# Performance work log

Hardware: AMD Instinct MI355X
Metric: run time of the kernel (lower is better)

Reference implementation:

```python
import jax, jax.numpy as jnp
import numpy as np

N, E, F_IN, C, H = 50000, 800000, 256, 128, 2
NEG_SLOPE = 0.2


def setup_inputs() -> dict:
    key = jax.random.key(0)
    ks = jax.random.split(key, 8)
    x = jax.random.normal(ks[0], (N, F_IN), dtype=jnp.float32)
    edge_index = jax.random.randint(ks[1], (2, E), 0, N, dtype=jnp.int64)
    # GATConv params (PyG: lin weight [H*C, F_IN], att_src/att_dst [H, C], bias [H*C])
    s_lin = 1.0 / np.sqrt(F_IN)
    W = jax.random.uniform(ks[2], (H * C, F_IN), minval=-s_lin, maxval=s_lin, dtype=jnp.float32)
    att_src = jax.random.normal(ks[3], (H, C), dtype=jnp.float32) * 0.1
    att_dst = jax.random.normal(ks[4], (H, C), dtype=jnp.float32) * 0.1
    bias = jnp.zeros((H * C,), dtype=jnp.float32)
    # trailing nn.Linear(H*C, C)
    s_l = 1.0 / np.sqrt(H * C)
    lin_w = jax.random.uniform(ks[5], (C, H * C), minval=-s_l, maxval=s_l, dtype=jnp.float32)
    lin_b = jax.random.uniform(ks[6], (C,), minval=-s_l, maxval=s_l, dtype=jnp.float32)
    return {"x": x, "edge_index": edge_index, "W": W, "att_src": att_src,
            "att_dst": att_dst, "bias": bias, "lin_w": lin_w, "lin_b": lin_b}


def _gat_forward(x, edge_index, W, att_src, att_dst, bias, lin_w, lin_b):
    # add self-loops (PyG default add_self_loops=True)
    loop = jnp.arange(N, dtype=edge_index.dtype)
    src = jnp.concatenate([edge_index[0], loop])  # [E+N]
    dst = jnp.concatenate([edge_index[1], loop])  # [E+N]

    h = (x @ W.T).reshape(N, H, C)                # [N, H, C]
    a_src = jnp.einsum('nhc,hc->nh', h, att_src)  # [N, H]
    a_dst = jnp.einsum('nhc,hc->nh', h, att_dst)  # [N, H]

    e = a_src[src] + a_dst[dst]                   # [E+N, H]
    e = jnp.where(e > 0, e, NEG_SLOPE * e)        # LeakyReLU(0.2)

    # softmax over edges grouped by destination node
    m = jax.ops.segment_max(e, dst, num_segments=N)          # [N, H]
    m = jnp.where(jnp.isfinite(m), m, 0.0)
    ex = jnp.exp(e - jax.lax.stop_gradient(m)[dst])
    denom = jax.ops.segment_sum(ex, dst, num_segments=N)     # [N, H]
    alpha = ex / jnp.maximum(denom[dst], 1e-16)               # [E+N, H]

    msg = h[src] * alpha[:, :, None]                          # [E+N, H, C]
    out = jax.ops.segment_sum(msg, dst, num_segments=N)       # [N, H, C]
    out = out.reshape(N, H * C) + bias

    out = jax.nn.elu(out)
    return out @ lin_w.T + lin_b                               # [N, C]


def reference(x, edge_index, W, att_src, att_dst, bias, lin_w, lin_b):
    return _gat_forward(x, edge_index, W, att_src, att_dst, bias, lin_w, lin_b)
```

## Files before the change

### kernel.cpp

```cpp
#include <hip/hip_runtime.h>
#include <hip/hip_fp16.h>
#include <math.h>

#define NN 50000
#define EE 800000
#define ET (EE + NN)
#define FIN 256
#define CCOUT 128
#define HH 2
#define HC 256
#define NEG 0.2f

#define NB_EDGE ((ET + 255) / 256)
#define NB_SCAN ((NN + 255) / 256)
#define NB_XPREP (NN / 4)

#define PREP_W_BLOCKS 64
#define PREP_LW_BLOCKS 32
#define PREP_GRID (3 + PREP_W_BLOCKS + PREP_LW_BLOCKS)

typedef __attribute__((ext_vector_type(8))) short short8;
typedef __attribute__((ext_vector_type(4))) float floatx4;

__device__ __forceinline__ unsigned short f2bf(float f)
{
    union { float f; unsigned int u; } x; x.f = f;
    unsigned int r = x.u + 0x7fffu + ((x.u >> 16) & 1u);
    return (unsigned short)(r >> 16);
}
__device__ __forceinline__ float bf2f(unsigned short u)
{
    union { unsigned int u; float f; } x; x.u = ((unsigned int)u) << 16;
    return x.f;
}
__device__ __forceinline__ float h2f_bits(unsigned short u)
{
    __half h = *(const __half*)&u;
    return __half2float(h);
}

__device__ __forceinline__ int load_idx(const int* ei32, int is64, int pos)
{
    return is64 ? ei32[2 * pos] : ei32[pos];
}

__global__ __launch_bounds__(256) void prep_kernel(const float* __restrict__ W,
                                                   const float* __restrict__ att_s,
                                                   const float* __restrict__ att_d,
                                                   const float* __restrict__ lin_w,
                                                   const int* __restrict__ ei32,
                                                   float* __restrict__ was,
                                                   float* __restrict__ wad,
                                                   unsigned short* __restrict__ Wb,
                                                   unsigned short* __restrict__ linwb,
                                                   int* __restrict__ flag)
{
    int b = blockIdx.x, t = threadIdx.x;
    if (b == 0) {
        if (t < 64) {
            int v = ei32[2 * t + 1];
            unsigned long long m = __ballot(v != 0);
            if (t == 0) *flag = (m == 0ull) ? 1 : 0;
        }
    } else if (b <= 2) {
        int hd = b - 1;
        float as = 0.f, ad = 0.f;
        for (int c = 0; c < CCOUT; c++) {
            float wv = W[(size_t)(hd * CCOUT + c) * FIN + t];
            as += att_s[hd * CCOUT + c] * wv;
            ad += att_d[hd * CCOUT + c] * wv;
        }
        was[hd * FIN + t] = as;
        wad[hd * FIN + t] = ad;
    } else if (b < 3 + PREP_W_BLOCKS) {
        int i = (b - 3) * 256 + t;
        float4 v = *(const float4*)(W + (size_t)i * 4);
        ushort4 o;
        o.x = f2bf(v.x); o.y = f2bf(v.y); o.z = f2bf(v.z); o.w = f2bf(v.w);
        *(ushort4*)(Wb + (size_t)i * 4) = o;
    } else {
        int i = (b - 3 - PREP_W_BLOCKS) * 256 + t;
        float4 v = *(const float4*)(lin_w + (size_t)i * 4);
        ushort4 o;
        o.x = f2bf(v.x); o.y = f2bf(v.y); o.z = f2bf(v.z); o.w = f2bf(v.w);
        *(ushort4*)(linwb + (size_t)i * 4) = o;
    }
}

__global__ __launch_bounds__(256) void xprep_count_kernel(const float* __restrict__ x,
                                                          const float* __restrict__ was,
                                                          const float* __restrict__ wad,
                                                          unsigned short* __restrict__ xb,
                                                          float* __restrict__ a_s,
                                                          float* __restrict__ a_d,
                                                          const int* __restrict__ ei32,
                                                          const int* __restrict__ flag,
                                                          int* __restrict__ deg,
                                                          int* __restrict__ eord)
{
    int b = blockIdx.x, t = threadIdx.x;
    if (b < NB_XPREP) {
        int w = t >> 6, l = t & 63;
        int n = b * 4 + w;
        float4 xv = *(const float4*)(x + (size_t)n * FIN + l * 4);
        ushort4 xs;
        xs.x = f2bf(xv.x); xs.y = f2bf(xv.y); xs.z = f2bf(xv.z); xs.w = f2bf(xv.w);
        *(ushort4*)(xb + (size_t)n * FIN + l * 4) = xs;

        float4 s0 = *(const float4*)(was + l * 4);
        float4 s1 = *(const float4*)(was + FIN + l * 4);
        float4 d0 = *(const float4*)(wad + l * 4);
        float4 d1 = *(const float4*)(wad + FIN + l * 4);
        float vs0 = xv.x * s0.x + xv.y * s0.y + xv.z * s0.z + xv.w * s0.w;
        float vs1 = xv.x * s1.x + xv.y * s1.y + xv.z * s1.z + xv.w * s1.w;
        float vd0 = xv.x * d0.x + xv.y * d0.y + xv.z * d0.z + xv.w * d0.w;
        float vd1 = xv.x * d1.x + xv.y * d1.y + xv.z * d1.z + xv.w * d1.w;
#pragma unroll
        for (int off = 32; off > 0; off >>= 1) {
            vs0 += __shfl_down(vs0, off);
            vs1 += __shfl_down(vs1, off);
            vd0 += __shfl_down(vd0, off);
            vd1 += __shfl_down(vd1, off);
        }
        if (l == 0) {
            a_s[n * 2 + 0] = vs0; a_s[n * 2 + 1] = vs1;
            a_d[n * 2 + 0] = vd0; a_d[n * 2 + 1] = vd1;
        }
    } else {
        int e = (b - NB_XPREP) * 256 + t;
        if (e < ET) {
            int is64 = *flag;
            int d = (e < EE) ? load_idx(ei32, is64, EE + e) : (e - EE);
            eord[e] = atomicAdd(&deg[d], 1);
        }
    }
}

template <bool ADD_BIAS, bool OUT_BF16>
__global__ __launch_bounds__(256) void gemm_mfma(const unsigned short* __restrict__ A,
                                                 const unsigned short* __restrict__ B,
                                                 const float* __restrict__ bias,
                                                 void* __restrict__ Cout,
                                                 int M, int N, int K)
{
    const int LDT = 40;
    __shared__ unsigned short As[128 * LDT];
    __shared__ unsigned short Bs[128 * LDT];

    int tid = threadIdx.x;
    int wave = tid >> 6, lane = tid & 63;
    int wr = wave >> 1, wc = wave & 1;
    int quad = lane >> 4, l16 = lane & 15;
    int bm0 = blockIdx.x * 128;
    int bn0 = blockIdx.y * 128;

    floatx4 acc[4][4] = {};

    for (int kk = 0; kk < K; kk += 32) {
#pragma unroll
        for (int p = 0; p < 2; p++) {
            int idx = p * 256 + tid;
            int row = idx >> 2, seg = idx & 3;
            int grow = bm0 + row; if (grow >= M) grow = M - 1;
            uint4 va = *(const uint4*)(A + (size_t)grow * K + kk + seg * 8);
            *(uint4*)(&As[row * LDT + seg * 8]) = va;
            uint4 vb = *(const uint4*)(B + (size_t)(bn0 + row) * K + kk + seg * 8);
            *(uint4*)(&Bs[row * LDT + seg * 8]) = vb;
        }
        __syncthreads();

        short8 af[4], bfr[4];
#pragma unroll
        for (int mi = 0; mi < 4; mi++)
            af[mi] = *(const short8*)(&As[(wr * 64 + mi * 16 + l16) * LDT + quad * 8]);
#pragma unroll
        for (int ni = 0; ni < 4; ni++)
            bfr[ni] = *(const short8*)(&Bs[(wc * 64 + ni * 16 + l16) * LDT + quad * 8]);
#pragma unroll
        for (int mi = 0; mi < 4; mi++)
#pragma unroll
            for (int ni = 0; ni < 4; ni++)
                acc[mi][ni] = __builtin_amdgcn_mfma_f32_16x16x32_bf16(af[mi], bfr[ni], acc[mi][ni], 0, 0, 0);
        __syncthreads();
    }

#pragma unroll
    for (int mi = 0; mi < 4; mi++) {
#pragma unroll
        for (int ni = 0; ni < 4; ni++) {
            int col = bn0 + wc * 64 + ni * 16 + l16;
#pragma unroll
            for (int r = 0; r < 4; r++) {
                int row = bm0 + wr * 64 + mi * 16 + quad * 4 + r;
                if (row < M) {
                    float v = acc[mi][ni][r];
                    if (ADD_BIAS) v += bias[col];
                    if (OUT_BF16)
                        ((unsigned short*)Cout)[(size_t)row * N + col] = f2bf(v);
                    else
                        ((float*)Cout)[(size_t)row * N + col] = v;
                }
            }
        }
    }
}

__global__ __launch_bounds__(256) void scan1(const int* __restrict__ deg,
                                             int* __restrict__ tmp, int* __restrict__ bsum)
{
    __shared__ int s[256];
    int i = blockIdx.x * 256 + threadIdx.x;
    int v = (i < NN) ? deg[i] : 0;
    s[threadIdx.x] = v;
    __syncthreads();
    for (int off = 1; off < 256; off <<= 1) {
        int add = (threadIdx.x >= off) ? s[threadIdx.x - off] : 0;
        __syncthreads();
        s[threadIdx.x] += add;
        __syncthreads();
    }
    if (i < NN) tmp[i] = s[threadIdx.x];
    if (threadIdx.x == 255) bsum[blockIdx.x] = s[255];
}

__global__ __launch_bounds__(256) void scan2(int* __restrict__ bsum)
{
    __shared__ int s[256];
    int t = threadIdx.x;
    int v = (t < NB_SCAN) ? bsum[t] : 0;
    s[t] = v;
    __syncthreads();
    for (int off = 1; off < 256; off <<= 1) {
        int add = (t >= off) ? s[t - off] : 0;
        __syncthreads();
        s[t] += add;
        __syncthreads();
    }
    if (t < NB_SCAN) bsum[t] = s[t] - v;
}

__global__ __launch_bounds__(256) void scan3(const int* __restrict__ deg,
                                             const int* __restrict__ tmp,
                                             const int* __restrict__ bsum,
                                             int* __restrict__ rowstart)
{
    int i = blockIdx.x * 256 + threadIdx.x;
    if (i < NN) rowstart[i] = tmp[i] - deg[i] + bsum[blockIdx.x];
    if (i == 0) rowstart[NN] = ET;
}

__global__ void scatter_kernel(const int* __restrict__ ei32, const int* __restrict__ flag,
                               const int* __restrict__ eord,
                               const int* __restrict__ rowstart,
                               const float* __restrict__ a_s,
                               const float* __restrict__ a_d,
                               uint2* __restrict__ rec)
{
    int e = blockIdx.x * blockDim.x + threadIdx.x;
    if (e >= ET) return;
    int is64 = *flag;
    int s, d;
    if (e < EE) { s = load_idx(ei32, is64, e); d = load_idx(ei32, is64, EE + e); }
    else { s = d = e - EE; }
    float e0 = a_s[s * 2 + 0] + a_d[d * 2 + 0];
    float e1 = a_s[s * 2 + 1] + a_d[d * 2 + 1];
    e0 = e0 > 0.f ? e0 : NEG * e0;
    e1 = e1 > 0.f ? e1 : NEG * e1;
    __half2 hp = __floats2half2_rn(__expf(e0), __expf(e1));
    uint2 r;
    r.x = (unsigned int)s;
    r.y = *(unsigned int*)&hp;
    rec[rowstart[d] + eord[e]] = r;
}

__global__ __launch_bounds__(256) void agg5_kernel(const unsigned short* __restrict__ hb,
                                                   const int* __restrict__ rowstart,
                                                   const uint2* __restrict__ rec,
                                                   const float* __restrict__ bias,
                                                   unsigned short* __restrict__ aggb)
{
    int wave = threadIdx.x >> 6, lane = threadIdx.x & 63;
    int d = blockIdx.x * 4 + wave;
    int head = lane >> 5;
    int hshift = head << 4;
    int c = (lane & 31) * 4 + head * 128;
    int j0 = rowstart[d], j1 = rowstart[d + 1];

    float acc0 = 0.f, acc1 = 0.f, acc2 = 0.f, acc3 = 0.f, psum = 0.f;

    int j = j0;
    for (; j + 3 < j1; j += 4) {
        uint2 r0 = rec[j], r1 = rec[j + 1], r2 = rec[j + 2], r3 = rec[j + 3];
        float p0 = h2f_bits((unsigned short)(r0.y >> hshift));
        float p1 = h2f_bits((unsigned short)(r1.y >> hshift));
        float p2 = h2f_bits((unsigned short)(r2.y >> hshift));
        float p3 = h2f_bits((unsigned short)(r3.y >> hshift));
        psum += p0 + p1 + p2 + p3;
        uint2 h0 = *(const uint2*)(hb + (size_t)r0.x * HC + c);
        uint2 h1 = *(const uint2*)(hb + (size_t)r1.x * HC + c);
        uint2 h2 = *(const uint2*)(hb + (size_t)r2.x * HC + c);
        uint2 h3 = *(const uint2*)(hb + (size_t)r3.x * HC + c);
        acc0 += p0 * bf2f((unsigned short)h0.x) + p1 * bf2f((unsigned short)h1.x)
              + p2 * bf2f((unsigned short)h2.x) + p3 * bf2f((unsigned short)h3.x);
        acc1 += p0 * bf2f((unsigned short)(h0.x >> 16)) + p1 * bf2f((unsigned short)(h1.x >> 16))
              + p2 * bf2f((unsigned short)(h2.x >> 16)) + p3 * bf2f((unsigned short)(h3.x >> 16));
        acc2 += p0 * bf2f((unsigned short)h0.y) + p1 * bf2f((unsigned short)h1.y)
              + p2 * bf2f((unsigned short)h2.y) + p3 * bf2f((unsigned short)h3.y);
        acc3 += p0 * bf2f((unsigned short)(h0.y >> 16)) + p1 * bf2f((unsigned short)(h1.y >> 16))
              + p2 * bf2f((unsigned short)(h2.y >> 16)) + p3 * bf2f((unsigned short)(h3.y >> 16));
    }
    for (; j < j1; j++) {
        uint2 r0 = rec[j];
        float p0 = h2f_bits((unsigned short)(r0.y >> hshift));
        psum += p0;
        uint2 h0 = *(const uint2*)(hb + (size_t)r0.x * HC + c);
        acc0 += p0 * bf2f((unsigned short)h0.x);
        acc1 += p0 * bf2f((unsigned short)(h0.x >> 16));
        acc2 += p0 * bf2f((unsigned short)h0.y);
        acc3 += p0 * bf2f((unsigned short)(h0.y >> 16));
    }

    float inv = 1.f / fmaxf(psum, 1e-16f);
    float v0 = acc0 * inv + bias[c + 0];
    float v1 = acc1 * inv + bias[c + 1];
    float v2 = acc2 * inv + bias[c + 2];
    float v3 = acc3 * inv + bias[c + 3];
    v0 = v0 > 0.f ? v0 : expm1f(v0);
    v1 = v1 > 0.f ? v1 : expm1f(v1);
    v2 = v2 > 0.f ? v2 : expm1f(v2);
    v3 = v3 > 0.f ? v3 : expm1f(v3);
    ushort4 o;
    o.x = f2bf(v0); o.y = f2bf(v1); o.z = f2bf(v2); o.w = f2bf(v3);
    *(ushort4*)(aggb + (size_t)d * HC + c) = o;
}

extern "C" void kernel_launch(void* const* d_in, const int* in_sizes, int n_in,
                              void* d_out, int out_size, void* d_ws, size_t ws_size,
                              hipStream_t stream)
{
    const float* x       = (const float*)d_in[0];
    const int*   ei32    = (const int*)d_in[1];
    const float* W       = (const float*)d_in[2];
    const float* att_src = (const float*)d_in[3];
    const float* att_dst = (const float*)d_in[4];
    const float* bias    = (const float*)d_in[5];
    const float* lin_w   = (const float*)d_in[6];
    const float* lin_b   = (const float*)d_in[7];
    float* out = (float*)d_out;

    char* ws = (char*)d_ws;
    size_t off = 0;
    auto alloc = [&](size_t bytes) -> void* {
        void* p = ws + off;
        off += (bytes + 255) & ~(size_t)255;
        return p;
    };

    int*   deg    = (int*)alloc((size_t)NN * 4);
    size_t zero_bytes = off;

    int*   flag     = (int*)alloc(256);
    int*   tmp      = (int*)alloc((size_t)NN * 4);
    int*   bsum     = (int*)alloc(1024);
    int*   rowstart = (int*)alloc((size_t)(NN + 1) * 4);
    int*   eord     = (int*)alloc((size_t)ET * 4);
    float* was      = (float*)alloc((size_t)HH * FIN * 4);
    float* wad      = (float*)alloc((size_t)HH * FIN * 4);
    float* a_s      = (float*)alloc((size_t)NN * 2 * 4);
    float* a_d      = (float*)alloc((size_t)NN * 2 * 4);
    uint2* rec      = (uint2*)alloc((size_t)ET * 8);
    unsigned short* xb     = (unsigned short*)alloc((size_t)NN * FIN * 2);
    unsigned short* Wb     = (unsigned short*)alloc((size_t)HC * FIN * 2);
    unsigned short* linwb  = (unsigned short*)alloc((size_t)CCOUT * HC * 2);
    unsigned short* hb     = (unsigned short*)alloc((size_t)NN * HC * 2);
    unsigned short* aggb   = (unsigned short*)alloc((size_t)NN * HC * 2);

    hipMemsetAsync(d_ws, 0, zero_bytes, stream);

    prep_kernel<<<PREP_GRID, 256, 0, stream>>>(W, att_src, att_dst, lin_w, ei32,
                                               was, wad, Wb, linwb, flag);

    xprep_count_kernel<<<NB_XPREP + NB_EDGE, 256, 0, stream>>>(x, was, wad, xb, a_s, a_d,
                                                               ei32, flag, deg, eord);

    scan1<<<NB_SCAN, 256, 0, stream>>>(deg, tmp, bsum);
    scan2<<<1, 256, 0, stream>>>(bsum);
    scan3<<<NB_SCAN, 256, 0, stream>>>(deg, tmp, bsum, rowstart);

    scatter_kernel<<<NB_EDGE, 256, 0, stream>>>(ei32, flag, eord, rowstart, a_s, a_d, rec);

    dim3 g1((NN + 127) / 128, HC / 128);
    gemm_mfma<false, true><<<g1, 256, 0, stream>>>(xb, Wb, nullptr, hb, NN, HC, FIN);

    agg5_kernel<<<NN / 4, 256, 0, stream>>>(hb, rowstart, rec, bias, aggb);

    dim3 g2((NN + 127) / 128, CCOUT / 128);
    gemm_mfma<true, false><<<g2, 256, 0, stream>>>(aggb, linwb, lin_b, out, NN, CCOUT, HC);
}
```

Baseline: 275.8 us.

## Split edges across half-waves in aggregation and merge scan passes

The aggregation kernel now has each half-wave cover the full 256-channel row with 16-byte loads. The two halves take alternating edges and combine their partial sums with a cross-lane shuffle, so each edge costs fewer, wider gathers and more loads are in flight per wave. Separately, the second and third prefix-scan kernels are fused: each block reduces the preceding block sums itself, which removes one kernel launch at the cost of redundant small reductions. The new agg epilogue runs on only half the lanes and adds shuffle overhead.

New measurement: 278.9 us. About the same (+1.1%).

```diff
diff --git a/kernel.cpp b/kernel.cpp
--- a/kernel.cpp
+++ b/kernel.cpp
@@ -31,6 +31,16 @@
 __device__ __forceinline__ float bf2f(unsigned short u)
 {
     union { unsigned int u; float f; } x; x.u = ((unsigned int)u) << 16;
+    return x.f;
+}
+__device__ __forceinline__ float bf_lo(unsigned int u)
+{
+    union { unsigned int u; float f; } x; x.u = u << 16;
+    return x.f;
+}
+__device__ __forceinline__ float bf_hi(unsigned int u)
+{
+    union { unsigned int u; float f; } x; x.u = u & 0xffff0000u;
     return x.f;
 }
 __device__ __forceinline__ float h2f_bits(unsigned short u)
@@ -223,29 +233,24 @@
     if (threadIdx.x == 255) bsum[blockIdx.x] = s[255];
 }
 
-__global__ __launch_bounds__(256) void scan2(int* __restrict__ bsum)
+__global__ __launch_bounds__(256) void scan23(const int* __restrict__ deg,
+                                              const int* __restrict__ tmp,
+                                              const int* __restrict__ bsum,
+                                              int* __restrict__ rowstart)
 {
     __shared__ int s[256];
-    int t = threadIdx.x;
-    int v = (t < NB_SCAN) ? bsum[t] : 0;
+    int b = blockIdx.x, t = threadIdx.x;
+    int v = (t < NB_SCAN && t < b) ? bsum[t] : 0;
     s[t] = v;
     __syncthreads();
-    for (int off = 1; off < 256; off <<= 1) {
-        int add = (t >= off) ? s[t - off] : 0;
+#pragma unroll
+    for (int off = 128; off > 0; off >>= 1) {
+        if (t < off) s[t] += s[t + off];
         __syncthreads();
-        s[t] += add;
-        __syncthreads();
-    }
-    if (t < NB_SCAN) bsum[t] = s[t] - v;
-}
-
-__global__ __launch_bounds__(256) void scan3(const int* __restrict__ deg,
-                                             const int* __restrict__ tmp,
-                                             const int* __restrict__ bsum,
-                                             int* __restrict__ rowstart)
-{
-    int i = blockIdx.x * 256 + threadIdx.x;
-    if (i < NN) rowstart[i] = tmp[i] - deg[i] + bsum[blockIdx.x];
+    }
+    int offset = s[0];
+    int i = b * 256 + t;
+    if (i < NN) rowstart[i] = tmp[i] - deg[i] + offset;
     if (i == 0) rowstart[NN] = ET;
 }
 
@@ -273,7 +278,7 @@
     rec[rowstart[d] + eord[e]] = r;
 }
 
-__global__ __launch_bounds__(256) void agg5_kernel(const unsigned short* __restrict__ hb,
+__global__ __launch_bounds__(256) void agg6_kernel(const unsigned short* __restrict__ hb,
                                                    const int* __restrict__ rowstart,
                                                    const uint2* __restrict__ rec,
                                                    const float* __restrict__ bias,
@@ -281,57 +286,85 @@
 {
     int wave = threadIdx.x >> 6, lane = threadIdx.x & 63;
     int d = blockIdx.x * 4 + wave;
-    int head = lane >> 5;
-    int hshift = head << 4;
-    int c = (lane & 31) * 4 + head * 128;
+    int half = lane >> 5;
+    int l = lane & 31;
+    int hshift = (l >> 4) << 4;
+    int c = l * 8;
     int j0 = rowstart[d], j1 = rowstart[d + 1];
 
-    float acc0 = 0.f, acc1 = 0.f, acc2 = 0.f, acc3 = 0.f, psum = 0.f;
-
-    int j = j0;
-    for (; j + 3 < j1; j += 4) {
-        uint2 r0 = rec[j], r1 = rec[j + 1], r2 = rec[j + 2], r3 = rec[j + 3];
+    float a0 = 0.f, a1 = 0.f, a2 = 0.f, a3 = 0.f;
+    float a4 = 0.f, a5 = 0.f, a6 = 0.f, a7 = 0.f;
+    float psum = 0.f;
+
+    int j = j0 + half;
+    for (; j + 2 < j1; j += 4) {
+        uint2 r0 = rec[j], r1 = rec[j + 2];
         float p0 = h2f_bits((unsigned short)(r0.y >> hshift));
         float p1 = h2f_bits((unsigned short)(r1.y >> hshift));
-        float p2 = h2f_bits((unsigned short)(r2.y >> hshift));
-        float p3 = h2f_bits((unsigned short)(r3.y >> hshift));
-        psum += p0 + p1 + p2 + p3;
-        uint2 h0 = *(const uint2*)(hb + (size_t)r0.x * HC + c);
-        uint2 h1 = *(const uint2*)(hb + (size_t)r1.x * HC + c);
-        uint2 h2 = *(const uint2*)(hb + (size_t)r2.x * HC + c);
-        uint2 h3 = *(const uint2*)(hb + (size_t)r3.x * HC + c);
-        acc0 += p0 * bf2f((unsigned short)h0.x) + p1 * bf2f((unsigned short)h1.x)
-              + p2 * bf2f((unsigned short)h2.x) + p3 * bf2f((unsigned short)h3.x);
-        acc1 += p0 * bf2f((unsigned short)(h0.x >> 16)) + p1 * bf2f((unsigned short)(h1.x >> 16))
-              + p2 * bf2f((unsigned short)(h2.x >> 16)) + p3 * bf2f((unsigned short)(h3.x >> 16));
-        acc2 += p0 * bf2f((unsigned short)h0.y) + p1 * bf2f((unsigned short)h1.y)
-              + p2 * bf2f((unsigned short)h2.y) + p3 * bf2f((unsigned short)h3.y);
-        acc3 += p0 * bf2f((unsigned short)(h0.y >> 16)) + p1 * bf2f((unsigned short)(h1.y >> 16))
-              + p2 * bf2f((unsigned short)(h2.y >> 16)) + p3 * bf2f((unsigned short)(h3.y >> 16));
-    }
-    for (; j < j1; j++) {
+        psum += p0 + p1;
+        uint4 h0 = *(const uint4*)(hb + (size_t)r0.x * HC + c);
+        uint4 h1 = *(const uint4*)(hb + (size_t)r1.x * HC + c);
+        a0 += p0 * bf_lo(h0.x) + p1 * bf_lo(h1.x);
+        a1 += p0 * bf_hi(h0.x) + p1 * bf_hi(h1.x);
+        a2 += p0 * bf_lo(h0.y) + p1 * bf_lo(h1.y);
+        a3 += p0 * bf_hi(h0.y) + p1 * bf_hi(h1.y);
+        a4 += p0 * bf_lo(h0.z) + p1 * bf_lo(h1.z);
+        a5 += p0 * bf_hi(h0.z) + p1 * bf_hi(h1.z);
+        a6 += p0 * bf_lo(h0.w) + p1 * bf_lo(h1.w);
+        a7 += p0 * bf_hi(h0.w) + p1 * bf_hi(h1.w);
+    }
+    for (; j < j1; j += 2) {
         uint2 r0 = rec[j];
         float p0 = h2f_bits((unsigned short)(r0.y >> hshift));
         psum += p0;
-        uint2 h0 = *(const uint2*)(hb + (size_t)r0.x * HC + c);
-        acc0 += p0 * bf2f((unsigned short)h0.x);
-        acc1 += p0 * bf2f((unsigned short)(h0.x >> 16));
-        acc2 += p0 * bf2f((unsigned short)h0.y);
-        acc3 += p0 * bf2f((unsigned short)(h0.y >> 16));
-    }
-
-    float inv = 1.f / fmaxf(psum, 1e-16f);
-    float v0 = acc0 * inv + bias[c + 0];
-    float v1 = acc1 * inv + bias[c + 1];
-    float v2 = acc2 * inv + bias[c + 2];
-    float v3 = acc3 * inv + bias[c + 3];
-    v0 = v0 > 0.f ? v0 : expm1f(v0);
-    v1 = v1 > 0.f ? v1 : expm1f(v1);
-    v2 = v2 > 0.f ? v2 : expm1f(v2);
-    v3 = v3 > 0.f ? v3 : expm1f(v3);
-    ushort4 o;
-    o.x = f2bf(v0); o.y = f2bf(v1); o.z = f2bf(v2); o.w = f2bf(v3);
-    *(ushort4*)(aggb + (size_t)d * HC + c) = o;
+        uint4 h0 = *(const uint4*)(hb + (size_t)r0.x * HC + c);
+        a0 += p0 * bf_lo(h0.x);
+        a1 += p0 * bf_hi(h0.x);
+        a2 += p0 * bf_lo(h0.y);
+        a3 += p0 * bf_hi(h0.y);
+        a4 += p0 * bf_lo(h0.z);
+        a5 += p0 * bf_hi(h0.z);
+        a6 += p0 * bf_lo(h0.w);
+        a7 += p0 * bf_hi(h0.w);
+    }
+
+    a0 += __shfl_xor(a0, 32);
+    a1 += __shfl_xor(a1, 32);
+    a2 += __shfl_xor(a2, 32);
+    a3 += __shfl_xor(a3, 32);
+    a4 += __shfl_xor(a4, 32);
+    a5 += __shfl_xor(a5, 32);
+    a6 += __shfl_xor(a6, 32);
+    a7 += __shfl_xor(a7, 32);
+    psum += __shfl_xor(psum, 32);
+
+    if (half == 0) {
+        float inv = 1.f / fmaxf(psum, 1e-16f);
+        float4 b0 = *(const float4*)(bias + c);
+        float4 b1 = *(const float4*)(bias + c + 4);
+        float v0 = a0 * inv + b0.x;
+        float v1 = a1 * inv + b0.y;
+        float v2 = a2 * inv + b0.z;
+        float v3 = a3 * inv + b0.w;
+        float v4 = a4 * inv + b1.x;
+        float v5 = a5 * inv + b1.y;
+        float v6 = a6 * inv + b1.z;
+        float v7 = a7 * inv + b1.w;
+        v0 = v0 > 0.f ? v0 : expm1f(v0);
+        v1 = v1 > 0.f ? v1 : expm1f(v1);
+        v2 = v2 > 0.f ? v2 : expm1f(v2);
+        v3 = v3 > 0.f ? v3 : expm1f(v3);
+        v4 = v4 > 0.f ? v4 : expm1f(v4);
+        v5 = v5 > 0.f ? v5 : expm1f(v5);
+        v6 = v6 > 0.f ? v6 : expm1f(v6);
+        v7 = v7 > 0.f ? v7 : expm1f(v7);
+        uint4 o;
+        o.x = (unsigned int)f2bf(v0) | ((unsigned int)f2bf(v1) << 16);
+        o.y = (unsigned int)f2bf(v2) | ((unsigned int)f2bf(v3) << 16);
+        o.z = (unsigned int)f2bf(v4) | ((unsigned int)f2bf(v5) << 16);
+        o.w = (unsigned int)f2bf(v6) | ((unsigned int)f2bf(v7) << 16);
+        *(uint4*)(aggb + (size_t)d * HC + c) = o;
+    }
 }
 
 extern "C" void kernel_launch(void* const* d_in, const int* in_sizes, int n_in,
@@ -384,15 +417,14 @@
                                                                ei32, flag, deg, eord);
 
     scan1<<<NB_SCAN, 256, 0, stream>>>(deg, tmp, bsum);
-    scan2<<<1, 256, 0, stream>>>(bsum);
-    scan3<<<NB_SCAN, 256, 0, stream>>>(deg, tmp, bsum, rowstart);
+    scan23<<<NB_SCAN, 256, 0, stream>>>(deg, tmp, bsum, rowstart);
 
     scatter_kernel<<<NB_EDGE, 256, 0, stream>>>(ei32, flag, eord, rowstart, a_s, a_d, rec);
 
     dim3 g1((NN + 127) / 128, HC / 128);
     gemm_mfma<false, true><<<g1, 256, 0, stream>>>(xb, Wb, nullptr, hb, NN, HC, FIN);
 
-    agg5_kernel<<<NN / 4, 256, 0, stream>>>(hb, rowstart, rec, bias, aggb);
+    agg6_kernel<<<NN / 4, 256, 0, stream>>>(hb, rowstart, rec, bias, aggb);
 
     dim3 g2((NN + 127) / 128, CCOUT / 128);
     gemm_mfma<true, false><<<g2, 256, 0, stream>>>(aggb, linwb, lin_b, out, NN, CCOUT, HC);
```
